# Optimization experiments

Hardware: AMD Instinct MI355X
Metric: run time of the kernel (lower is better)

Reference implementation:

```python
import jax, jax.numpy as jnp
import numpy as np

D_IN, D_HIDDEN, DT_RANK = 768, 16, 48


def setup_inputs() -> dict:
    key = jax.random.key(0)
    ks = jax.random.split(key, 6)
    b, l, d, n, r = 2, 2048, D_IN, D_HIDDEN, DT_RANK
    p = 3 * n + 2 * d + 2 * r  # x_proj output width = 1680
    x = jax.random.normal(ks[0], (b, l, d), jnp.float32)
    z = jax.random.normal(ks[1], (b, d, l), jnp.float32)
    # A_log = log(repeat(arange(1, n+1), 'n -> d n'))
    A_log = jnp.log(jnp.broadcast_to(jnp.arange(1, n + 1, dtype=jnp.float32), (d, n)))
    D = jnp.ones((d,), jnp.float32)
    W_xproj = jax.random.normal(ks[2], (p, d), jnp.float32) / np.sqrt(d)
    W_dt = jax.random.normal(ks[3], (d, r), jnp.float32) / np.sqrt(r)
    # dt bias init: inverse-softplus of dt ~ LogUniform(1e-3, 1e-1)
    dt = jnp.exp(jax.random.uniform(ks[4], (d,)) * (np.log(0.1) - np.log(0.001)) + np.log(0.001))
    dt = jnp.clip(dt, 1e-4)
    b_dt = dt + jnp.log(-jnp.expm1(-dt))
    return dict(x=x, z=z, A_log=A_log, D=D, W_xproj=W_xproj, W_dt=W_dt, b_dt=b_dt)


def reference(x, z, A_log, D, W_xproj, W_dt, b_dt):
    b, l, d = x.shape
    n = A_log.shape[1]
    r = W_dt.shape[1]
    A = -jnp.exp(A_log)                      # (d, n)
    proj = x @ W_xproj.T                     # (b, l, 3n + 2d + 2r)
    Bm = proj[..., :n]                       # (b, l, n)  input matrix B
    Cm = proj[..., 2 * n:3 * n]              # (b, l, n)  output matrix C
    dt = proj[..., 3 * n + 2 * d:3 * n + 2 * d + r]   # (b, l, r)
    # NOTE: source adds dt_proj bias via the Linear AND again via delta_bias -> 2*b_dt
    delta = jax.nn.softplus(dt @ W_dt.T + 2.0 * b_dt)  # (b, l, d)
    dA = jnp.exp(delta[..., None] * A)                  # (b, l, d, n)
    dBu = (delta * x)[..., None] * Bm[:, :, None, :]    # (b, l, d, n)

    def step(h, inp):
        dA_t, dBu_t, C_t = inp
        h = dA_t * h + dBu_t                 # (b, d, n)
        return h, jnp.einsum('bdn,bn->bd', h, C_t)

    h0 = jnp.zeros((b, d, n), x.dtype)
    _, ys = jax.lax.scan(step, h0, (jnp.swapaxes(dA, 0, 1), jnp.swapaxes(dBu, 0, 1), jnp.swapaxes(Cm, 0, 1)))
    y = jnp.swapaxes(ys, 0, 1) + x * D       # (b, l, d)  + skip D*u
    zl = jnp.swapaxes(z, 1, 2)               # z is (b, d, l) -> (b, l, d)
    return y * (zl * jax.nn.sigmoid(zl))     # gate with silu(z)
```

## Files before the change

### kernel.cpp

```cpp
#include <hip/hip_runtime.h>
#include <math.h>

#define BATCH 2
#define LSEQ  2048
#define DIM   768
#define NST   16
#define RDT   48
#define BL    (BATCH*LSEQ)
#define NCHUNK 16
#define CLEN   (LSEQ/NCHUNK)
#define NPACK  (CLEN/4)
#define LP4    (LSEQ/4)
#define L2E    1.4426950408889634f

typedef __attribute__((ext_vector_type(8))) short short8;
typedef __attribute__((ext_vector_type(4))) float float4e;

__device__ __forceinline__ ushort f2bf(float f) {
    union { float f; unsigned u; } v; v.f = f;
    unsigned u = v.u;
    u += 0x7fffu + ((u >> 16) & 1u);
    return (ushort)(u >> 16);
}

template <int CTRL>
__device__ __forceinline__ float dpp_add(float v) {
    const int s = __builtin_amdgcn_update_dpp(__float_as_int(v), __float_as_int(v),
                                              CTRL, 0xF, 0xF, false);
    return v + __int_as_float(s);
}

__global__ __launch_bounds__(256) void pack_kernel(
        const float* __restrict__ x, const float* __restrict__ Wx,
        float* __restrict__ xT, ushort* __restrict__ Wbf) {
    if (blockIdx.y == DIM / 64) {
        const int blk = blockIdx.z * 32 + blockIdx.x;
        for (int idx = blk * 256 + threadIdx.x; idx < 80 * DIM; idx += 64 * 256) {
            const int j = idx / DIM;
            const int k = idx - j * DIM;
            const int row = (j < 16) ? j : ((j < 32) ? (j + 16) : (j + 1552));
            Wbf[idx] = f2bf(Wx[(size_t)row * DIM + k]);
        }
        return;
    }
    __shared__ float tile[64 * 65];
    const int r0 = blockIdx.x * 64;
    const int c0 = blockIdx.y * 64;
    const int b  = blockIdx.z;
    const int tid = threadIdx.x;
    {
        const int c4 = tid & 15, rb = tid >> 4;
        #pragma unroll
        for (int rr = 0; rr < 4; ++rr) {
            const int row = rr * 16 + rb;
            const float4 v = *(const float4*)(x + ((size_t)b * LSEQ + r0 + row) * DIM + c0 + c4 * 4);
            tile[(c4 * 4 + 0) * 65 + row] = v.x;
            tile[(c4 * 4 + 1) * 65 + row] = v.y;
            tile[(c4 * 4 + 2) * 65 + row] = v.z;
            tile[(c4 * 4 + 3) * 65 + row] = v.w;
        }
    }
    __syncthreads();
    {
        const int t4 = tid & 15, dq = tid >> 4;
        #pragma unroll
        for (int pass = 0; pass < 4; ++pass) {
            const int dd = pass * 16 + dq;
            float4 v;
            v.x = tile[dd * 65 + t4 * 4 + 0];
            v.y = tile[dd * 65 + t4 * 4 + 1];
            v.z = tile[dd * 65 + t4 * 4 + 2];
            v.w = tile[dd * 65 + t4 * 4 + 3];
            *(float4*)(xT + ((size_t)b * DIM + c0 + dd) * LSEQ + r0 + t4 * 4) = v;
        }
    }
}

__global__ __launch_bounds__(320) void proj_gemm_kernel(
        const float* __restrict__ x, const ushort* __restrict__ Wbf,
        float* __restrict__ Bpk, float* __restrict__ Cpk,
        float* __restrict__ dtpT) {
    const int m0   = blockIdx.x * 16;
    const int nt   = threadIdx.x >> 6;
    const int lane = threadIdx.x & 63;
    const int col  = lane & 15;
    const int quad = lane >> 4;

    const float* A  = x + (size_t)(m0 + col) * DIM + quad * 8;
    const short* Bw = (const short*)Wbf + (size_t)(nt * 16 + col) * DIM + quad * 8;

    float4e acc = {};
    #pragma unroll 4
    for (int kk = 0; kk < 24; ++kk) {
        const float4 a0 = *(const float4*)(A + kk * 32);
        const float4 a1 = *(const float4*)(A + kk * 32 + 4);
        short8 a;
        a[0] = (short)f2bf(a0.x); a[1] = (short)f2bf(a0.y);
        a[2] = (short)f2bf(a0.z); a[3] = (short)f2bf(a0.w);
        a[4] = (short)f2bf(a1.x); a[5] = (short)f2bf(a1.y);
        a[6] = (short)f2bf(a1.z); a[7] = (short)f2bf(a1.w);
        const short8 bf = *(const short8*)(Bw + kk * 32);
        acc = __builtin_amdgcn_mfma_f32_16x16x32_bf16(a, bf, acc, 0, 0, 0);
    }

    const int b  = m0 >> 11;
    const int t0 = m0 & 2047;
    if (nt == 0) {
        ((float4*)Bpk)[((size_t)(b * LP4 + (t0 >> 2) + quad)) * NST + col] = *(float4*)&acc;
    } else if (nt == 1) {
        ((float4*)Cpk)[((size_t)(b * LP4 + (t0 >> 2) + quad)) * NST + col] = *(float4*)&acc;
    } else {
        const int r = (nt - 2) * 16 + col;
        *(float4*)(dtpT + ((size_t)(b * RDT + r)) * LSEQ + t0 + quad * 4) = *(float4*)&acc;
    }
}

__global__ __launch_bounds__(256) void scan_kernel(
        const float* __restrict__ xT, const float* __restrict__ A_log,
        const float* __restrict__ Dp,
        const float* __restrict__ Bpk, const float* __restrict__ Cpk,
        const float* __restrict__ dtpT, const float* __restrict__ Wdt,
        const float* __restrict__ bdt, float* __restrict__ yv) {
    __shared__ float sdel[LSEQ];
    __shared__ float sP[NCHUNK][NST];
    __shared__ float sq[NCHUNK][NST];
    __shared__ float sw[RDT];

    const int tid = threadIdx.x;
    const int ch = blockIdx.x;
    const int b = ch / DIM;
    const int d = ch % DIM;
    const size_t row = (size_t)ch * LSEQ;

    if (tid < RDT) sw[tid] = Wdt[(size_t)d * RDT + tid];
    __syncthreads();

    {
        const float bb = 2.0f * bdt[d];
        const float* dbase = dtpT + (size_t)b * RDT * LSEQ;
        #pragma unroll
        for (int i = 0; i < 2; ++i) {
            const int idx = tid + 256 * i;
            float4 acc = make_float4(bb, bb, bb, bb);
            #pragma unroll 3
            for (int k4 = 0; k4 < RDT / 4; ++k4) {
                const float4 wv = ((const float4*)sw)[k4];
                #pragma unroll
                for (int j = 0; j < 4; ++j) {
                    const int k = k4 * 4 + j;
                    const float wk = (j == 0) ? wv.x : (j == 1) ? wv.y : (j == 2) ? wv.z : wv.w;
                    const float4 v = ((const float4*)(dbase + (size_t)k * LSEQ))[idx];
                    acc.x = fmaf(v.x, wk, acc.x);
                    acc.y = fmaf(v.y, wk, acc.y);
                    acc.z = fmaf(v.z, wk, acc.z);
                    acc.w = fmaf(v.w, wk, acc.w);
                }
            }
            float4 sp;
            sp.x = (acc.x > 20.f) ? acc.x : __logf(1.f + __expf(acc.x));
            sp.y = (acc.y > 20.f) ? acc.y : __logf(1.f + __expf(acc.y));
            sp.z = (acc.z > 20.f) ? acc.z : __logf(1.f + __expf(acc.z));
            sp.w = (acc.w > 20.f) ? acc.w : __logf(1.f + __expf(acc.w));
            ((float4*)sdel)[idx] = sp;
        }
    }
    __syncthreads();

    const int g = tid >> 4;
    const int n = tid & 15;
    const float Aln2 = -__expf(A_log[d * NST + n]) * L2E;
    const float4* Bg = (const float4*)Bpk + ((size_t)(b * LP4 + g * NPACK) * NST + n);
    const float4* Cg = (const float4*)Cpk + ((size_t)(b * LP4 + g * NPACK) * NST + n);
    const float4* xr = (const float4*)(xT + row) + g * NPACK;

    {
        float h = 0.f, Ptot = 1.f;
        float4 Bn_ = Bg[0], xn_ = xr[0];
        #pragma unroll 4
        for (int p = 0; p < NPACK; ++p) {
            const float4 B4 = Bn_, x4 = xn_;
            if (p < NPACK - 1) { Bn_ = Bg[(p + 1) * NST]; xn_ = xr[p + 1]; }
            const float4 dl = ((const float4*)sdel)[g * NPACK + p];
            const float u0 = dl.x * x4.x * B4.x, u1 = dl.y * x4.y * B4.y;
            const float u2 = dl.z * x4.z * B4.z, u3 = dl.w * x4.w * B4.w;
            const float e0  = __builtin_amdgcn_exp2f(Aln2 * dl.x);
            const float dA1 = __builtin_amdgcn_exp2f(Aln2 * dl.y);
            const float dA2 = __builtin_amdgcn_exp2f(Aln2 * dl.z);
            const float dA3 = __builtin_amdgcn_exp2f(Aln2 * dl.w);
            float s = u0;
            s = fmaf(dA1, s, u1); s = fmaf(dA2, s, u2); s = fmaf(dA3, s, u3);
            const float E3 = ((e0 * dA1) * (dA2 * dA3));
            h = fmaf(E3, h, s);
            Ptot *= E3;
        }
        sP[g][n] = Ptot;
        sq[g][n] = h;
    }
    __syncthreads();

    {
        float Pc = sP[g][n], qc = sq[g][n];
        #pragma unroll
        for (int s = 1; s < NCHUNK; s <<= 1) {
            float Pp = 1.f, qp = 0.f;
            if (g >= s) { Pp = sP[g - s][n]; qp = sq[g - s][n]; }
            __syncthreads();
            qc = fmaf(Pc, qp, qc);
            Pc *= Pp;
            sP[g][n] = Pc; sq[g][n] = qc;
            __syncthreads();
        }
    }

    {
        float h = (g == 0) ? 0.f : sq[g - 1][n];
        const float Dd = Dp[d];
        float4 Bn_ = Bg[0], Cn_ = Cg[0], xn_ = xr[0];
        #pragma unroll 4
        for (int p = 0; p < NPACK; ++p) {
            const float4 B4 = Bn_, C4 = Cn_, x4 = xn_;
            if (p < NPACK - 1) { Bn_ = Bg[(p + 1) * NST]; Cn_ = Cg[(p + 1) * NST]; xn_ = xr[p + 1]; }
            const float4 dl = ((const float4*)sdel)[g * NPACK + p];
            const float u0 = dl.x * x4.x * B4.x, u1 = dl.y * x4.y * B4.y;
            const float u2 = dl.z * x4.z * B4.z, u3 = dl.w * x4.w * B4.w;
            const float E0  = __builtin_amdgcn_exp2f(Aln2 * dl.x);
            const float dA1 = __builtin_amdgcn_exp2f(Aln2 * dl.y);
            const float dA2 = __builtin_amdgcn_exp2f(Aln2 * dl.z);
            const float dA3 = __builtin_amdgcn_exp2f(Aln2 * dl.w);
            const float E1 = E0 * dA1, E2 = E1 * dA2, E3 = E2 * dA3;
            const float s0 = u0;
            const float s1 = fmaf(dA1, s0, u1);
            const float s2 = fmaf(dA2, s1, u2);
            const float s3 = fmaf(dA3, s2, u3);
            const float h0 = fmaf(E0, h, s0);
            const float h1 = fmaf(E1, h, s1);
            const float h2 = fmaf(E2, h, s2);
            const float h3 = fmaf(E3, h, s3);
            h = h3;
            float p0 = h0 * C4.x, p1 = h1 * C4.y, p2 = h2 * C4.z, p3 = h3 * C4.w;
            p0 = dpp_add<0xB1>(p0); p0 = dpp_add<0x4E>(p0);
            p1 = dpp_add<0xB1>(p1); p1 = dpp_add<0x4E>(p1);
            p2 = dpp_add<0xB1>(p2); p2 = dpp_add<0x4E>(p2);
            p3 = dpp_add<0xB1>(p3); p3 = dpp_add<0x4E>(p3);
            float v = (n & 1) ? ((n & 2) ? p3 : p1) : ((n & 2) ? p2 : p0);
            v = dpp_add<0x124>(v);
            v = dpp_add<0x128>(v);
            if (n < 4) {
                const float xc = (n == 0) ? x4.x : (n == 1) ? x4.y : (n == 2) ? x4.z : x4.w;
                yv[row + g * CLEN + 4 * p + n] = fmaf(xc, Dd, v);
            }
        }
    }
}

__global__ __launch_bounds__(256) void xpose_out_kernel(
        const float* __restrict__ yv, const float* __restrict__ z,
        float* __restrict__ out) {
    __shared__ float tile[64 * 65];
    const int r0 = blockIdx.x * 64;
    const int c0 = blockIdx.y * 64;
    const int b  = blockIdx.z;
    const int tid = threadIdx.x;
    {
        const int c4 = tid & 15, rb = tid >> 4;
        #pragma unroll
        for (int rr = 0; rr < 4; ++rr) {
            const int row = rr * 16 + rb;
            const size_t gidx = ((size_t)b * DIM + r0 + row) * LSEQ + c0 + c4 * 4;
            const float4 v = *(const float4*)(yv + gidx);
            const float4 zv = *(const float4*)(z + gidx);
            tile[(c4 * 4 + 0) * 65 + row] = v.x * zv.x / (1.f + __expf(-zv.x));
            tile[(c4 * 4 + 1) * 65 + row] = v.y * zv.y / (1.f + __expf(-zv.y));
            tile[(c4 * 4 + 2) * 65 + row] = v.z * zv.z / (1.f + __expf(-zv.z));
            tile[(c4 * 4 + 3) * 65 + row] = v.w * zv.w / (1.f + __expf(-zv.w));
        }
    }
    __syncthreads();
    {
        const int t4 = tid & 15, dq = tid >> 4;
        #pragma unroll
        for (int pass = 0; pass < 4; ++pass) {
            const int ll = pass * 16 + dq;
            float4 v;
            v.x = tile[ll * 65 + t4 * 4 + 0];
            v.y = tile[ll * 65 + t4 * 4 + 1];
            v.z = tile[ll * 65 + t4 * 4 + 2];
            v.w = tile[ll * 65 + t4 * 4 + 3];
            *(float4*)(out + ((size_t)b * LSEQ + c0 + ll) * DIM + r0 + t4 * 4) = v;
        }
    }
}

extern "C" void kernel_launch(void* const* d_in, const int* in_sizes, int n_in,
                              void* d_out, int out_size, void* d_ws, size_t ws_size,
                              hipStream_t stream) {
    const float* x     = (const float*)d_in[0];
    const float* z     = (const float*)d_in[1];
    const float* A_log = (const float*)d_in[2];
    const float* D     = (const float*)d_in[3];
    const float* Wx    = (const float*)d_in[4];
    const float* Wdt   = (const float*)d_in[5];
    const float* bdt   = (const float*)d_in[6];
    float* out = (float*)d_out;

    float* ws    = (float*)d_ws;
    float* Bpk   = ws;
    float* Cpk   = Bpk + (size_t)BATCH * LP4 * NST * 4;
    float* dtpT  = Cpk + (size_t)BATCH * LP4 * NST * 4;
    float* xT    = dtpT + (size_t)BATCH * RDT * LSEQ;
    float* yv    = xT;
    ushort* Wbf  = (ushort*)(xT + (size_t)BATCH * DIM * LSEQ);

    hipLaunchKernelGGL(pack_kernel, dim3(LSEQ / 64, DIM / 64 + 1, BATCH), dim3(256), 0, stream,
                       x, Wx, xT, Wbf);
    hipLaunchKernelGGL(proj_gemm_kernel, dim3(BL / 16), dim3(320), 0, stream,
                       x, Wbf, Bpk, Cpk, dtpT);
    hipLaunchKernelGGL(scan_kernel, dim3(BATCH * DIM), dim3(256), 0, stream,
                       xT, A_log, D, Bpk, Cpk, dtpT, Wdt, bdt, yv);
    hipLaunchKernelGGL(xpose_out_kernel, dim3(DIM / 64, LSEQ / 64, BATCH), dim3(256), 0, stream,
                       yv, z, out);
}
```

Measured before the change: 165.2 us.

## Fuse x transpose and dt projection into GEMM kernel, double scan chunks

Moves the dt_proj matmul and softplus out of the per-channel scan kernel into the projection GEMM, where they run as bf16 MFMA and write a transposed delta array. The separate x transpose kernel is removed by having one wave in the GEMM write x transposed with strided scalar stores. The scan kernel now just loads precomputed delta into padded shared memory and uses 32 chunks with 512 threads for more parallelism. The cost is a large extra delta buffer in global memory, uncoalesced transposed stores of x, and bf16 rounding in the dt projection.

```diff
diff --git a/kernel.cpp b/kernel.cpp
--- a/kernel.cpp
+++ b/kernel.cpp
@@ -7,8 +7,9 @@
 #define NST   16
 #define RDT   48
 #define BL    (BATCH*LSEQ)
-#define NCHUNK 16
+#define NCHUNK 32
 #define CLEN   (LSEQ/NCHUNK)
+#define CPAD   68
 #define NPACK  (CLEN/4)
 #define LP4    (LSEQ/4)
 #define L2E    1.4426950408889634f
@@ -30,61 +31,39 @@
     return v + __int_as_float(s);
 }
 
-__global__ __launch_bounds__(256) void pack_kernel(
-        const float* __restrict__ x, const float* __restrict__ Wx,
-        float* __restrict__ xT, ushort* __restrict__ Wbf) {
-    if (blockIdx.y == DIM / 64) {
-        const int blk = blockIdx.z * 32 + blockIdx.x;
-        for (int idx = blk * 256 + threadIdx.x; idx < 80 * DIM; idx += 64 * 256) {
-            const int j = idx / DIM;
-            const int k = idx - j * DIM;
-            const int row = (j < 16) ? j : ((j < 32) ? (j + 16) : (j + 1552));
-            Wbf[idx] = f2bf(Wx[(size_t)row * DIM + k]);
-        }
-        return;
-    }
-    __shared__ float tile[64 * 65];
-    const int r0 = blockIdx.x * 64;
-    const int c0 = blockIdx.y * 64;
-    const int b  = blockIdx.z;
-    const int tid = threadIdx.x;
-    {
-        const int c4 = tid & 15, rb = tid >> 4;
-        #pragma unroll
-        for (int rr = 0; rr < 4; ++rr) {
-            const int row = rr * 16 + rb;
-            const float4 v = *(const float4*)(x + ((size_t)b * LSEQ + r0 + row) * DIM + c0 + c4 * 4);
-            tile[(c4 * 4 + 0) * 65 + row] = v.x;
-            tile[(c4 * 4 + 1) * 65 + row] = v.y;
-            tile[(c4 * 4 + 2) * 65 + row] = v.z;
-            tile[(c4 * 4 + 3) * 65 + row] = v.w;
-        }
-    }
-    __syncthreads();
-    {
-        const int t4 = tid & 15, dq = tid >> 4;
-        #pragma unroll
-        for (int pass = 0; pass < 4; ++pass) {
-            const int dd = pass * 16 + dq;
-            float4 v;
-            v.x = tile[dd * 65 + t4 * 4 + 0];
-            v.y = tile[dd * 65 + t4 * 4 + 1];
-            v.z = tile[dd * 65 + t4 * 4 + 2];
-            v.w = tile[dd * 65 + t4 * 4 + 3];
-            *(float4*)(xT + ((size_t)b * DIM + c0 + dd) * LSEQ + r0 + t4 * 4) = v;
-        }
+__global__ __launch_bounds__(256) void wpack_kernel(
+        const float* __restrict__ Wx, const float* __restrict__ Wdt,
+        ushort* __restrict__ Wbf, ushort* __restrict__ Wdtbf) {
+    const int tid0 = blockIdx.x * 256 + threadIdx.x;
+    for (int i = tid0; i < 80 * DIM; i += gridDim.x * 256) {
+        const int j = i / DIM;
+        const int k = i - j * DIM;
+        const int row = (j < 16) ? j : ((j < 32) ? (j + 16) : (j + 1552));
+        Wbf[i] = f2bf(Wx[(size_t)row * DIM + k]);
+    }
+    for (int i = tid0; i < DIM * 64; i += gridDim.x * 256) {
+        const int dd = i >> 6;
+        const int k = i & 63;
+        Wdtbf[i] = (k < RDT) ? f2bf(Wdt[dd * RDT + k]) : (ushort)0;
     }
 }
 
 __global__ __launch_bounds__(320) void proj_gemm_kernel(
         const float* __restrict__ x, const ushort* __restrict__ Wbf,
+        const ushort* __restrict__ Wdtbf, const float* __restrict__ bdt,
         float* __restrict__ Bpk, float* __restrict__ Cpk,
-        float* __restrict__ dtpT) {
+        float* __restrict__ deltaT, float* __restrict__ xT) {
+    __shared__ float dtp_s[16 * 65];
     const int m0   = blockIdx.x * 16;
     const int nt   = threadIdx.x >> 6;
     const int lane = threadIdx.x & 63;
     const int col  = lane & 15;
     const int quad = lane >> 4;
+    const int b  = m0 >> 11;
+    const int t0 = m0 & 2047;
+
+    for (int i = threadIdx.x; i < 16 * 65; i += 320) dtp_s[i] = 0.f;
+    __syncthreads();
 
     const float* A  = x + (size_t)(m0 + col) * DIM + quad * 8;
     const short* Bw = (const short*)Wbf + (size_t)(nt * 16 + col) * DIM + quad * 8;
@@ -99,32 +78,64 @@
         a[2] = (short)f2bf(a0.z); a[3] = (short)f2bf(a0.w);
         a[4] = (short)f2bf(a1.x); a[5] = (short)f2bf(a1.y);
         a[6] = (short)f2bf(a1.z); a[7] = (short)f2bf(a1.w);
+        if (nt == 0) {
+            const int dbase = kk * 32 + quad * 8;
+            float* xc = xT + ((size_t)(b * DIM + dbase)) * LSEQ + t0 + col;
+            xc[0 * LSEQ] = a0.x; xc[1 * LSEQ] = a0.y;
+            xc[2 * LSEQ] = a0.z; xc[3 * LSEQ] = a0.w;
+            xc[4 * LSEQ] = a1.x; xc[5 * LSEQ] = a1.y;
+            xc[6 * LSEQ] = a1.z; xc[7 * LSEQ] = a1.w;
+        }
         const short8 bf = *(const short8*)(Bw + kk * 32);
         acc = __builtin_amdgcn_mfma_f32_16x16x32_bf16(a, bf, acc, 0, 0, 0);
     }
 
-    const int b  = m0 >> 11;
-    const int t0 = m0 & 2047;
     if (nt == 0) {
         ((float4*)Bpk)[((size_t)(b * LP4 + (t0 >> 2) + quad)) * NST + col] = *(float4*)&acc;
     } else if (nt == 1) {
         ((float4*)Cpk)[((size_t)(b * LP4 + (t0 >> 2) + quad)) * NST + col] = *(float4*)&acc;
     } else {
-        const int r = (nt - 2) * 16 + col;
-        *(float4*)(dtpT + ((size_t)(b * RDT + r)) * LSEQ + t0 + quad * 4) = *(float4*)&acc;
-    }
-}
-
-__global__ __launch_bounds__(256) void scan_kernel(
+        #pragma unroll
+        for (int r = 0; r < 4; ++r)
+            dtp_s[(quad * 4 + r) * 65 + (nt - 2) * 16 + col] = acc[r];
+    }
+    __syncthreads();
+
+    short8 da0, da1;
+    #pragma unroll
+    for (int j = 0; j < 8; ++j) {
+        da0[j] = (short)f2bf(dtp_s[col * 65 + quad * 8 + j]);
+        da1[j] = (short)f2bf(dtp_s[col * 65 + 32 + quad * 8 + j]);
+    }
+    for (int dt = nt; dt < 48; dt += 5) {
+        const int d0 = dt * 16;
+        const short8 b0 = *(const short8*)((const short*)Wdtbf + (size_t)(d0 + col) * 64 + quad * 8);
+        const short8 b1 = *(const short8*)((const short*)Wdtbf + (size_t)(d0 + col) * 64 + 32 + quad * 8);
+        float4e dacc = {};
+        dacc = __builtin_amdgcn_mfma_f32_16x16x32_bf16(da0, b0, dacc, 0, 0, 0);
+        dacc = __builtin_amdgcn_mfma_f32_16x16x32_bf16(da1, b1, dacc, 0, 0, 0);
+        const float bb = 2.0f * bdt[d0 + col];
+        float4 sp;
+        {
+            const float v0 = dacc[0] + bb, v1 = dacc[1] + bb;
+            const float v2 = dacc[2] + bb, v3 = dacc[3] + bb;
+            sp.x = (v0 > 20.f) ? v0 : __logf(1.f + __expf(v0));
+            sp.y = (v1 > 20.f) ? v1 : __logf(1.f + __expf(v1));
+            sp.z = (v2 > 20.f) ? v2 : __logf(1.f + __expf(v2));
+            sp.w = (v3 > 20.f) ? v3 : __logf(1.f + __expf(v3));
+        }
+        *(float4*)(deltaT + ((size_t)(b * DIM + d0 + col)) * LSEQ + t0 + quad * 4) = sp;
+    }
+}
+
+__global__ __launch_bounds__(512) void scan_kernel(
         const float* __restrict__ xT, const float* __restrict__ A_log,
         const float* __restrict__ Dp,
         const float* __restrict__ Bpk, const float* __restrict__ Cpk,
-        const float* __restrict__ dtpT, const float* __restrict__ Wdt,
-        const float* __restrict__ bdt, float* __restrict__ yv) {
-    __shared__ float sdel[LSEQ];
+        const float* __restrict__ deltaT, float* __restrict__ yv) {
+    __shared__ float sdel[NCHUNK * CPAD];
     __shared__ float sP[NCHUNK][NST];
     __shared__ float sq[NCHUNK][NST];
-    __shared__ float sw[RDT];
 
     const int tid = threadIdx.x;
     const int ch = blockIdx.x;
@@ -132,37 +143,9 @@
     const int d = ch % DIM;
     const size_t row = (size_t)ch * LSEQ;
 
-    if (tid < RDT) sw[tid] = Wdt[(size_t)d * RDT + tid];
-    __syncthreads();
-
-    {
-        const float bb = 2.0f * bdt[d];
-        const float* dbase = dtpT + (size_t)b * RDT * LSEQ;
-        #pragma unroll
-        for (int i = 0; i < 2; ++i) {
-            const int idx = tid + 256 * i;
-            float4 acc = make_float4(bb, bb, bb, bb);
-            #pragma unroll 3
-            for (int k4 = 0; k4 < RDT / 4; ++k4) {
-                const float4 wv = ((const float4*)sw)[k4];
-                #pragma unroll
-                for (int j = 0; j < 4; ++j) {
-                    const int k = k4 * 4 + j;
-                    const float wk = (j == 0) ? wv.x : (j == 1) ? wv.y : (j == 2) ? wv.z : wv.w;
-                    const float4 v = ((const float4*)(dbase + (size_t)k * LSEQ))[idx];
-                    acc.x = fmaf(v.x, wk, acc.x);
-                    acc.y = fmaf(v.y, wk, acc.y);
-                    acc.z = fmaf(v.z, wk, acc.z);
-                    acc.w = fmaf(v.w, wk, acc.w);
-                }
-            }
-            float4 sp;
-            sp.x = (acc.x > 20.f) ? acc.x : __logf(1.f + __expf(acc.x));
-            sp.y = (acc.y > 20.f) ? acc.y : __logf(1.f + __expf(acc.y));
-            sp.z = (acc.z > 20.f) ? acc.z : __logf(1.f + __expf(acc.z));
-            sp.w = (acc.w > 20.f) ? acc.w : __logf(1.f + __expf(acc.w));
-            ((float4*)sdel)[idx] = sp;
-        }
+    {
+        const float4 dv4 = ((const float4*)(deltaT + row))[tid];
+        ((float4*)sdel)[(tid >> 4) * (CPAD / 4) + (tid & 15)] = dv4;
     }
     __syncthreads();
 
@@ -172,6 +155,7 @@
     const float4* Bg = (const float4*)Bpk + ((size_t)(b * LP4 + g * NPACK) * NST + n);
     const float4* Cg = (const float4*)Cpk + ((size_t)(b * LP4 + g * NPACK) * NST + n);
     const float4* xr = (const float4*)(xT + row) + g * NPACK;
+    const float* dchunk = sdel + g * CPAD;
 
     {
         float h = 0.f, Ptot = 1.f;
@@ -180,7 +164,7 @@
         for (int p = 0; p < NPACK; ++p) {
             const float4 B4 = Bn_, x4 = xn_;
             if (p < NPACK - 1) { Bn_ = Bg[(p + 1) * NST]; xn_ = xr[p + 1]; }
-            const float4 dl = ((const float4*)sdel)[g * NPACK + p];
+            const float4 dl = *(const float4*)(dchunk + 4 * p);
             const float u0 = dl.x * x4.x * B4.x, u1 = dl.y * x4.y * B4.y;
             const float u2 = dl.z * x4.z * B4.z, u3 = dl.w * x4.w * B4.w;
             const float e0  = __builtin_amdgcn_exp2f(Aln2 * dl.x);
@@ -220,7 +204,7 @@
         for (int p = 0; p < NPACK; ++p) {
             const float4 B4 = Bn_, C4 = Cn_, x4 = xn_;
             if (p < NPACK - 1) { Bn_ = Bg[(p + 1) * NST]; Cn_ = Cg[(p + 1) * NST]; xn_ = xr[p + 1]; }
-            const float4 dl = ((const float4*)sdel)[g * NPACK + p];
+            const float4 dl = *(const float4*)(dchunk + 4 * p);
             const float u0 = dl.x * x4.x * B4.x, u1 = dl.y * x4.y * B4.y;
             const float u2 = dl.z * x4.z * B4.z, u3 = dl.w * x4.w * B4.w;
             const float E0  = __builtin_amdgcn_exp2f(Aln2 * dl.x);
@@ -303,20 +287,21 @@
     const float* bdt   = (const float*)d_in[6];
     float* out = (float*)d_out;
 
-    float* ws    = (float*)d_ws;
-    float* Bpk   = ws;
-    float* Cpk   = Bpk + (size_t)BATCH * LP4 * NST * 4;
-    float* dtpT  = Cpk + (size_t)BATCH * LP4 * NST * 4;
-    float* xT    = dtpT + (size_t)BATCH * RDT * LSEQ;
-    float* yv    = xT;
-    ushort* Wbf  = (ushort*)(xT + (size_t)BATCH * DIM * LSEQ);
-
-    hipLaunchKernelGGL(pack_kernel, dim3(LSEQ / 64, DIM / 64 + 1, BATCH), dim3(256), 0, stream,
-                       x, Wx, xT, Wbf);
+    float* ws     = (float*)d_ws;
+    float* Bpk    = ws;
+    float* Cpk    = Bpk + (size_t)BATCH * LP4 * NST * 4;
+    float* deltaT = Cpk + (size_t)BATCH * LP4 * NST * 4;
+    float* xT     = deltaT + (size_t)BATCH * DIM * LSEQ;
+    float* yv     = xT;
+    ushort* Wbf   = (ushort*)(xT + (size_t)BATCH * DIM * LSEQ);
+    ushort* Wdtbf = Wbf + (size_t)80 * DIM;
+
+    hipLaunchKernelGGL(wpack_kernel, dim3(64), dim3(256), 0, stream,
+                       Wx, Wdt, Wbf, Wdtbf);
     hipLaunchKernelGGL(proj_gemm_kernel, dim3(BL / 16), dim3(320), 0, stream,
-                       x, Wbf, Bpk, Cpk, dtpT);
-    hipLaunchKernelGGL(scan_kernel, dim3(BATCH * DIM), dim3(256), 0, stream,
-                       xT, A_log, D, Bpk, Cpk, dtpT, Wdt, bdt, yv);
+                       x, Wbf, Wdtbf, bdt, Bpk, Cpk, deltaT, xT);
+    hipLaunchKernelGGL(scan_kernel, dim3(BATCH * DIM), dim3(512), 0, stream,
+                       xT, A_log, D, Bpk, Cpk, deltaT, yv);
     hipLaunchKernelGGL(xpose_out_kernel, dim3(DIM / 64, LSEQ / 64, BATCH), dim3(256), 0, stream,
                        yv, z, out);
 }
```

After: 152.5 us. 7.7% less time.
